# Performance work log

Hardware: AMD Instinct MI355X
Metric: run time of the kernel (lower is better)

The kernel has to match this reference:

```python
import jax, jax.numpy as jnp
import numpy as np

B, N, K = 4, 100000, 128
Q_MIN = 0.5
S_B = 1.0
POT_SCALE = 1.0
REP_SCALE = 1.0
BETA_SCALE = 1.0
E_WEIGHT = 1.0
POS_WEIGHT = 1.0
TIME_WEIGHT = 1.0
HUBER_D = 2.0


def setup_inputs() -> dict:
    key = jax.random.key(0)
    ks = jax.random.split(key, 9)
    return {
        "beta": jax.random.uniform(ks[0], (B, N), dtype=jnp.float32),
        "ccoords": jax.random.normal(ks[1], (B, N, 2), dtype=jnp.float32),
        "pred_energy": jax.random.uniform(ks[2], (B, N), dtype=jnp.float32),
        "pred_pos": jax.random.normal(ks[3], (B, N, 2), dtype=jnp.float32),
        "pred_time": jax.random.uniform(ks[4], (B, N), dtype=jnp.float32),
        "t_energy": jax.random.uniform(ks[5], (B, N), dtype=jnp.float32),
        "t_pos": jax.random.normal(ks[6], (B, N, 2), dtype=jnp.float32),
        "t_time": jax.random.uniform(ks[7], (B, N), dtype=jnp.float32),
        "t_idx": jax.random.randint(ks[8], (B, N), 0, K + 1, dtype=jnp.int32),
    }


def _huber(x, d):
    a = jnp.abs(x)
    return jnp.where(a <= d, 0.5 * x * x, d * (a - 0.5 * d))


def _oc_loss(beta, ccoords, pred_energy, pred_pos, pred_time,
             t_energy, t_pos, t_time, t_idx):
    eps = 1e-4
    beta = jnp.clip(beta, eps, 1.0 - eps)
    q = jnp.arctanh(beta) ** 2 + Q_MIN                     # [B,N]

    obj = t_idx - 1                                        # -1 = noise, 0..K-1 = object id
    M = obj[:, :, None] == jnp.arange(K, dtype=jnp.int32)  # [B,N,K] bool membership
    Mf = M.astype(q.dtype)
    obj_exists = jnp.any(M, axis=1)                        # [B,K]
    exf = obj_exists.astype(q.dtype)

    # condensation point per object = member hit with max charge q (segment argmax)
    q_masked = jnp.where(M, q[:, :, None], -1.0)           # [B,N,K]
    alpha = jnp.argmax(q_masked, axis=1)                   # [B,K]
    x_alpha = jnp.take_along_axis(ccoords, alpha[:, :, None], axis=1)  # [B,K,2]
    q_alpha = jnp.take_along_axis(q, alpha, axis=1)        # [B,K]
    beta_alpha = jnp.take_along_axis(beta, alpha, axis=1)  # [B,K]

    # pairwise hit <-> condensation-point distances, [B,N,K]
    diff = ccoords[:, :, None, :] - x_alpha[:, None, :, :]
    dist = jnp.sqrt(jnp.sum(diff * diff, axis=-1) + 1e-12)

    qq = q[:, :, None] * q_alpha[:, None, :] * exf[:, None, :]
    v_att = qq * (dist * dist) * Mf
    v_rep = qq * jax.nn.relu(1.0 - dist) * (1.0 - Mf)
    n_tot = jnp.asarray(B * N, q.dtype)
    L_att = jnp.sum(v_att) / n_tot
    L_rep = jnp.sum(v_rep) / n_tot

    # beta loss: pull condensation-point betas to 1, suppress noise betas
    n_obj = jnp.maximum(jnp.sum(exf), 1.0)
    L_beta_obj = jnp.sum((1.0 - beta_alpha) * exf) / n_obj
    noise = (t_idx == 0).astype(q.dtype)
    L_noise = jnp.sum(beta * noise) / jnp.maximum(jnp.sum(noise), 1.0)
    L_beta = L_beta_obj + S_B * L_noise

    # payload losses, beta-weighted over non-noise hits
    p = (jnp.arctanh(beta) ** 2) * (1.0 - noise)           # [B,N]
    p_sum = jnp.maximum(jnp.sum(p), 1e-6)
    L_energy = jnp.sum(p * _huber(pred_energy - t_energy, HUBER_D)) / p_sum
    L_pos = jnp.sum(p * jnp.sum((pred_pos - t_pos) ** 2, axis=-1)) / p_sum
    L_time = jnp.sum(p * (pred_time - t_time) ** 2) / p_sum

    return (POT_SCALE * L_att + REP_SCALE * L_rep + BETA_SCALE * L_beta
            + E_WEIGHT * L_energy + POS_WEIGHT * L_pos + TIME_WEIGHT * L_time)


def reference(beta, ccoords, pred_energy, pred_pos, pred_time,
              t_energy, t_pos, t_time, t_idx):
    return _oc_loss(beta, ccoords, pred_energy, pred_pos, pred_time,
                    t_energy, t_pos, t_time, t_idx)
```

## Files before the change

kernel.cpp:

```cpp
#include <hip/hip_runtime.h>
#include <math.h>

#define BB 4
#define NN 100000
#define KK 128
#define HB 256
#define HH 4
#define GX ((NN + HB * HH - 1) / (HB * HH))
#define NBLK (GX * BB)


typedef float v2f __attribute__((ext_vector_type(2)));

#if __has_builtin(__builtin_elementwise_fma)
#define FMA2(a, b, c) __builtin_elementwise_fma((a), (b), (c))
#else
static __device__ __forceinline__ v2f fma2_(v2f a, v2f b, v2f c) {
    v2f r; r.x = __builtin_fmaf(a.x, b.x, c.x); r.y = __builtin_fmaf(a.y, b.y, c.y);
    return r;
}
#define FMA2 fma2_
#endif

#if __has_builtin(__builtin_elementwise_max)
#define MAX2(a, b) __builtin_elementwise_max((a), (b))
#else
static __device__ __forceinline__ v2f max2_(v2f a, v2f b) {
    v2f r; r.x = fmaxf(a.x, b.x); r.y = fmaxf(a.y, b.y);
    return r;
}
#define MAX2 max2_
#endif

__device__ __forceinline__ float clipb(float b) {
    return fminf(fmaxf(b, 1e-4f), 1.0f - 1e-4f);
}

__global__ void k_argmax(const float* __restrict__ beta,
                         const int* __restrict__ tidx,
                         unsigned long long* __restrict__ packed) {
    int b = blockIdx.y;
    __shared__ unsigned long long smax[KK];
    for (int t = threadIdx.x; t < KK; t += blockDim.x) smax[t] = 0ULL;
    __syncthreads();
    const float* betab = beta + b * NN;
    const int*   tib   = tidx + b * NN;
    for (int n = blockIdx.x * blockDim.x + threadIdx.x; n < NN;
         n += gridDim.x * blockDim.x) {
        int obj = tib[n] - 1;
        if (obj >= 0) {
            unsigned hi = __float_as_uint(clipb(betab[n]));
            unsigned long long key = ((unsigned long long)hi << 32) |
                                     (unsigned long long)(0xFFFFFFFFu - (unsigned)n);
            atomicMax(&smax[obj], key);
        }
    }
    __syncthreads();
    for (int t = threadIdx.x; t < KK; t += blockDim.x) {
        unsigned long long v = smax[t];
        if (v) atomicMax(&packed[b * KK + t], v);
    }
}

__global__ void __launch_bounds__(HB) k_main(
    const float*  __restrict__ beta, const float2* __restrict__ cc,
    const float*  __restrict__ pe,   const float2* __restrict__ pp,
    const float*  __restrict__ pt,   const float*  __restrict__ te,
    const float2* __restrict__ tp,   const float*  __restrict__ tt,
    const int*    __restrict__ tidx,
    const unsigned long long* __restrict__ packed,
    float* __restrict__ part) {
    int b = blockIdx.y;
    __shared__ v2f sox[KK / 2];
    __shared__ v2f soy[KK / 2];
    __shared__ v2f soq[KK / 2];
    __shared__ float sred[4][8];
    float* sax = (float*)sox;
    float* say = (float*)soy;
    float* saq = (float*)soq;

    if (threadIdx.x < KK) {
        unsigned long long v = packed[b * KK + threadIdx.x];
        float x = 0.f, y = 0.f, qz = 0.f;
        if (v) {
            unsigned n = 0xFFFFFFFFu - (unsigned)(v & 0xFFFFFFFFu);
            float ba = __uint_as_float((unsigned)(v >> 32));
            float at = atanhf(ba);
            float2 c = cc[b * NN + (int)n];
            x = c.x; y = c.y; qz = at * at + 0.5f;
        }
        sax[threadIdx.x] = x;
        say[threadIdx.x] = y;
        saq[threadIdx.x] = qz;
    }

    int base = blockIdx.x * (HB * HH) + threadIdx.x;
    bool vv[HH]; int ii[HH]; float2 ch[HH]; float rp[HH];
    v2f cx2[HH], cy2[HH];
    #pragma unroll
    for (int h = 0; h < HH; ++h) {
        int n = base + h * HB;
        vv[h] = n < NN;
        ii[h] = b * NN + (vv[h] ? n : 0);
        ch[h] = cc[ii[h]];
        cx2[h].x = ch[h].x; cx2[h].y = ch[h].x;
        cy2[h].x = ch[h].y; cy2[h].y = ch[h].y;
        rp[h] = 0.f;
    }
    __syncthreads();

    const v2f eps2 = {1e-12f, 1e-12f};
    const v2f one2 = {1.0f, 1.0f};
    const v2f zero2 = {0.0f, 0.0f};

    #pragma unroll 2
    for (int k2 = 0; k2 < KK / 2; ++k2) {
        v2f ox = sox[k2], oy = soy[k2], oq = soq[k2];
        #pragma unroll
        for (int h = 0; h < HH; ++h) {
            v2f dx = cx2[h] - ox;
            v2f dy = cy2[h] - oy;
            v2f s  = FMA2(dx, dx, FMA2(dy, dy, eps2));
            v2f d;
            d.x = __builtin_amdgcn_sqrtf(s.x);
            d.y = __builtin_amdgcn_sqrtf(s.y);
            v2f r = MAX2(one2 - d, zero2);
            rp[h] = fmaf(oq.x, r.x, rp[h]);
            rp[h] = fmaf(oq.y, r.y, rp[h]);
        }
    }

    float p_att = 0.f, p_rep = 0.f, p_nb = 0.f, p_nc = 0.f;
    float p_ps = 0.f, p_e = 0.f, p_pos = 0.f, p_tm = 0.f;

    #pragma unroll
    for (int h = 0; h < HH; ++h) {
        if (!vv[h]) continue;
        int   idx = ii[h];
        float rep = rp[h];
        float bc  = clipb(beta[idx]);
        float at  = atanhf(bc);
        float at2 = at * at;
        float q   = at2 + 0.5f;
        int   ti  = tidx[idx];
        int   obj = ti - 1;

        if (obj >= 0) {
            float ox = sax[obj], oy = say[obj], oqz = saq[obj];
            float dx = ch[h].x - ox, dy = ch[h].y - oy;
            float s = fmaf(dx, dx, fmaf(dy, dy, 1e-12f));
            float d = __builtin_amdgcn_sqrtf(s);
            rep   -= oqz * fmaxf(1.0f - d, 0.0f);
            p_att += q * (oqz * s);
        }
        p_rep += q * rep;

        if (ti == 0) {
            p_nb += bc;
            p_nc += 1.0f;
        } else {
            p_ps += at2;
            float de = pe[idx] - te[idx];
            float a  = fabsf(de);
            float hb = (a <= 2.0f) ? (0.5f * de * de) : (2.0f * (a - 1.0f));
            p_e  += at2 * hb;
            float2 ppv = pp[idx], tpv = tp[idx];
            float dpx = ppv.x - tpv.x, dpy = ppv.y - tpv.y;
            p_pos += at2 * (dpx * dpx + dpy * dpy);
            float dt = pt[idx] - tt[idx];
            p_tm += at2 * dt * dt;
        }
    }

    float vals[8] = {p_att, p_rep, p_nb, p_nc, p_ps, p_e, p_pos, p_tm};
    int lane = threadIdx.x & 63, wave = threadIdx.x >> 6;
    #pragma unroll
    for (int i = 0; i < 8; ++i) {
        float v = vals[i];
        #pragma unroll
        for (int off = 32; off > 0; off >>= 1) v += __shfl_down(v, off, 64);
        if (lane == 0) sred[wave][i] = v;
    }
    __syncthreads();
    if (threadIdx.x < 8) {
        float s = sred[0][threadIdx.x] + sred[1][threadIdx.x] +
                  sred[2][threadIdx.x] + sred[3][threadIdx.x];
        part[(b * GX + blockIdx.x) * 8 + threadIdx.x] = s;
    }
}

__global__ void __launch_bounds__(64) k_final(
    const float* __restrict__ part,
    const unsigned long long* __restrict__ packed,
    float* __restrict__ out) {
    int lane = threadIdx.x;

    float nobj = 0.f, sba = 0.f;
    for (int t = lane; t < BB * KK; t += 64) {
        unsigned long long v = packed[t];
        if (v) {
            nobj += 1.f;
            sba  += 1.0f - __uint_as_float((unsigned)(v >> 32));
        }
    }
    #pragma unroll
    for (int off = 32; off > 0; off >>= 1) {
        nobj += __shfl_xor(nobj, off, 64);
        sba  += __shfl_xor(sba, off, 64);
    }

    int comp = lane & 7;
    float v = 0.f;
    for (int r = lane >> 3; r < NBLK; r += 8)
        v += part[r * 8 + comp];
    v += __shfl_xor(v, 8, 64);
    v += __shfl_xor(v, 16, 64);
    v += __shfl_xor(v, 32, 64);
    float tot[8];
    #pragma unroll
    for (int c = 0; c < 8; ++c) tot[c] = __shfl(v, c, 64);

    if (lane == 0) {
        float inv_n  = 1.0f / (float)(BB * NN);
        float L_beta = sba / fmaxf(nobj, 1.0f) +
                       tot[2] / fmaxf(tot[3], 1.0f);
        float p_sum  = fmaxf(tot[4], 1e-6f);
        out[0] = tot[0] * inv_n + tot[1] * inv_n + L_beta +
                 (tot[5] + tot[6] + tot[7]) / p_sum;
    }
}

extern "C" void kernel_launch(void* const* d_in, const int* in_sizes, int n_in,
                              void* d_out, int out_size, void* d_ws, size_t ws_size,
                              hipStream_t stream) {
    const float*  beta = (const float*)d_in[0];
    const float2* cc   = (const float2*)d_in[1];
    const float*  pe   = (const float*)d_in[2];
    const float2* pp   = (const float2*)d_in[3];
    const float*  pt   = (const float*)d_in[4];
    const float*  te   = (const float*)d_in[5];
    const float2* tp   = (const float2*)d_in[6];
    const float*  tt   = (const float*)d_in[7];
    const int*    ti   = (const int*)d_in[8];

    unsigned long long* packed = (unsigned long long*)d_ws;
    float* part = (float*)((char*)d_ws + 4096);
    float* out  = (float*)d_out;

    hipMemsetAsync(packed, 0, 4096, stream);
    k_argmax<<<dim3(64, BB), 256, 0, stream>>>(beta, ti, packed);
    k_main<<<dim3(GX, BB), HB, 0, stream>>>(
        beta, cc, pe, pp, pt, te, tp, tt, ti, packed, part);
    k_final<<<1, 64, 0, stream>>>(part, packed, out);
}
```

Before: 120.1 us.

## Drop memset and final kernel via per-block argmax partials and last-block reduction

The argmax kernel now reads beta and t_idx with vector loads and writes per-block partial maxima instead of doing global atomics. That removes the memset, and the main kernel reduces the 32 partials itself. The separate final kernel is folded into the main kernel through a last-block-done atomic counter. HH rises to 7 with a fixed grid of 56 blocks per batch, giving fewer, larger blocks. The goal is less launch and memset overhead, at the cost of every main block redundantly reducing the partials and of lower parallelism.

Measured after the change: 118.4 us. About the same (-1.4%).

```diff
diff --git a/kernel.cpp b/kernel.cpp
--- a/kernel.cpp
+++ b/kernel.cpp
@@ -5,9 +5,10 @@
 #define NN 100000
 #define KK 128
 #define HB 256
-#define HH 4
-#define GX ((NN + HB * HH - 1) / (HB * HH))
+#define HH 7
+#define GX 56
 #define NBLK (GX * BB)
+#define PB 32
 
 
 typedef float v2f __attribute__((ext_vector_type(2)));
@@ -36,30 +37,35 @@
     return fminf(fmaxf(b, 1e-4f), 1.0f - 1e-4f);
 }
 
-__global__ void k_argmax(const float* __restrict__ beta,
-                         const int* __restrict__ tidx,
-                         unsigned long long* __restrict__ packed) {
+__device__ __forceinline__ unsigned long long mkkey(float bf, unsigned n) {
+    unsigned hi = __float_as_uint(clipb(bf));
+    return ((unsigned long long)hi << 32) |
+           (unsigned long long)(0xFFFFFFFFu - n);
+}
+
+__global__ void __launch_bounds__(256) k_argmax(
+    const float4* __restrict__ beta4, const int4* __restrict__ tidx4,
+    unsigned long long* __restrict__ pk_part, unsigned int* __restrict__ cnt) {
     int b = blockIdx.y;
     __shared__ unsigned long long smax[KK];
-    for (int t = threadIdx.x; t < KK; t += blockDim.x) smax[t] = 0ULL;
-    __syncthreads();
-    const float* betab = beta + b * NN;
-    const int*   tib   = tidx + b * NN;
-    for (int n = blockIdx.x * blockDim.x + threadIdx.x; n < NN;
-         n += gridDim.x * blockDim.x) {
-        int obj = tib[n] - 1;
-        if (obj >= 0) {
-            unsigned hi = __float_as_uint(clipb(betab[n]));
-            unsigned long long key = ((unsigned long long)hi << 32) |
-                                     (unsigned long long)(0xFFFFFFFFu - (unsigned)n);
-            atomicMax(&smax[obj], key);
-        }
-    }
-    __syncthreads();
-    for (int t = threadIdx.x; t < KK; t += blockDim.x) {
-        unsigned long long v = smax[t];
-        if (v) atomicMax(&packed[b * KK + t], v);
-    }
+    for (int t = threadIdx.x; t < KK; t += 256) smax[t] = 0ULL;
+    if (blockIdx.x == 0 && b == 0 && threadIdx.x == 0) *cnt = 0u;
+    __syncthreads();
+    const float4* b4 = beta4 + (size_t)b * (NN / 4);
+    const int4*   t4 = tidx4 + (size_t)b * (NN / 4);
+    for (int i = blockIdx.x * 256 + threadIdx.x; i < NN / 4; i += PB * 256) {
+        float4 bv = b4[i];
+        int4   tv = t4[i];
+        unsigned n0 = 4u * (unsigned)i;
+        if (tv.x > 0) atomicMax(&smax[tv.x - 1], mkkey(bv.x, n0));
+        if (tv.y > 0) atomicMax(&smax[tv.y - 1], mkkey(bv.y, n0 + 1));
+        if (tv.z > 0) atomicMax(&smax[tv.z - 1], mkkey(bv.z, n0 + 2));
+        if (tv.w > 0) atomicMax(&smax[tv.w - 1], mkkey(bv.w, n0 + 3));
+    }
+    __syncthreads();
+    if (threadIdx.x < KK)
+        pk_part[((size_t)b * PB + blockIdx.x) * KK + threadIdx.x] =
+            smax[threadIdx.x];
 }
 
 __global__ void __launch_bounds__(HB) k_main(
@@ -68,19 +74,30 @@
     const float*  __restrict__ pt,   const float*  __restrict__ te,
     const float2* __restrict__ tp,   const float*  __restrict__ tt,
     const int*    __restrict__ tidx,
-    const unsigned long long* __restrict__ packed,
-    float* __restrict__ part) {
+    const unsigned long long* __restrict__ pk_part,
+    unsigned long long* __restrict__ final_packed,
+    float* __restrict__ part, unsigned int* __restrict__ cnt,
+    float* __restrict__ out) {
     int b = blockIdx.y;
     __shared__ v2f sox[KK / 2];
     __shared__ v2f soy[KK / 2];
     __shared__ v2f soq[KK / 2];
     __shared__ float sred[4][8];
+    __shared__ unsigned s_last;
     float* sax = (float*)sox;
     float* say = (float*)soy;
     float* saq = (float*)soq;
 
     if (threadIdx.x < KK) {
-        unsigned long long v = packed[b * KK + threadIdx.x];
+        const unsigned long long* src =
+            pk_part + ((size_t)b * PB) * KK + threadIdx.x;
+        unsigned long long v = 0ULL;
+        #pragma unroll 8
+        for (int pb = 0; pb < PB; ++pb) {
+            unsigned long long u = src[(size_t)pb * KK];
+            v = (u > v) ? u : v;
+        }
+        if (blockIdx.x == 0) final_packed[b * KK + threadIdx.x] = v;
         float x = 0.f, y = 0.f, qz = 0.f;
         if (v) {
             unsigned n = 0xFFFFFFFFu - (unsigned)(v & 0xFFFFFFFFu);
@@ -95,16 +112,16 @@
     }
 
     int base = blockIdx.x * (HB * HH) + threadIdx.x;
-    bool vv[HH]; int ii[HH]; float2 ch[HH]; float rp[HH];
+    bool vv[HH]; int ii[HH]; float rp[HH];
     v2f cx2[HH], cy2[HH];
     #pragma unroll
     for (int h = 0; h < HH; ++h) {
         int n = base + h * HB;
         vv[h] = n < NN;
         ii[h] = b * NN + (vv[h] ? n : 0);
-        ch[h] = cc[ii[h]];
-        cx2[h].x = ch[h].x; cx2[h].y = ch[h].x;
-        cy2[h].x = ch[h].y; cy2[h].y = ch[h].y;
+        float2 c = cc[ii[h]];
+        cx2[h].x = c.x; cx2[h].y = c.x;
+        cy2[h].x = c.y; cy2[h].y = c.y;
         rp[h] = 0.f;
     }
     __syncthreads();
@@ -147,7 +164,7 @@
 
         if (obj >= 0) {
             float ox = sax[obj], oy = say[obj], oqz = saq[obj];
-            float dx = ch[h].x - ox, dy = ch[h].y - oy;
+            float dx = cx2[h].x - ox, dy = cy2[h].x - oy;
             float s = fmaf(dx, dx, fmaf(dy, dy, 1e-12f));
             float d = __builtin_amdgcn_sqrtf(s);
             rep   -= oqz * fmaxf(1.0f - d, 0.0f);
@@ -187,46 +204,53 @@
                   sred[2][threadIdx.x] + sred[3][threadIdx.x];
         part[(b * GX + blockIdx.x) * 8 + threadIdx.x] = s;
     }
-}
-
-__global__ void __launch_bounds__(64) k_final(
-    const float* __restrict__ part,
-    const unsigned long long* __restrict__ packed,
-    float* __restrict__ out) {
-    int lane = threadIdx.x;
-
-    float nobj = 0.f, sba = 0.f;
-    for (int t = lane; t < BB * KK; t += 64) {
-        unsigned long long v = packed[t];
-        if (v) {
-            nobj += 1.f;
-            sba  += 1.0f - __uint_as_float((unsigned)(v >> 32));
-        }
-    }
-    #pragma unroll
-    for (int off = 32; off > 0; off >>= 1) {
-        nobj += __shfl_xor(nobj, off, 64);
-        sba  += __shfl_xor(sba, off, 64);
-    }
-
-    int comp = lane & 7;
-    float v = 0.f;
-    for (int r = lane >> 3; r < NBLK; r += 8)
-        v += part[r * 8 + comp];
-    v += __shfl_xor(v, 8, 64);
-    v += __shfl_xor(v, 16, 64);
-    v += __shfl_xor(v, 32, 64);
-    float tot[8];
-    #pragma unroll
-    for (int c = 0; c < 8; ++c) tot[c] = __shfl(v, c, 64);
-
-    if (lane == 0) {
-        float inv_n  = 1.0f / (float)(BB * NN);
-        float L_beta = sba / fmaxf(nobj, 1.0f) +
-                       tot[2] / fmaxf(tot[3], 1.0f);
-        float p_sum  = fmaxf(tot[4], 1e-6f);
-        out[0] = tot[0] * inv_n + tot[1] * inv_n + L_beta +
-                 (tot[5] + tot[6] + tot[7]) / p_sum;
+    __syncthreads();
+
+    if (threadIdx.x == 0) {
+        __threadfence();
+        unsigned prev = atomicAdd(cnt, 1u);
+        s_last = (prev == (unsigned)(NBLK - 1)) ? 1u : 0u;
+    }
+    __syncthreads();
+    if (s_last) {
+        __threadfence();
+        if (threadIdx.x < 64) {
+            int flane = threadIdx.x;
+
+            float nobj = 0.f, sba = 0.f;
+            for (int t = flane; t < BB * KK; t += 64) {
+                unsigned long long v = final_packed[t];
+                if (v) {
+                    nobj += 1.f;
+                    sba  += 1.0f - __uint_as_float((unsigned)(v >> 32));
+                }
+            }
+            #pragma unroll
+            for (int off = 32; off > 0; off >>= 1) {
+                nobj += __shfl_xor(nobj, off, 64);
+                sba  += __shfl_xor(sba, off, 64);
+            }
+
+            int comp = flane & 7;
+            float v = 0.f;
+            for (int r = flane >> 3; r < NBLK; r += 8)
+                v += part[r * 8 + comp];
+            v += __shfl_xor(v, 8, 64);
+            v += __shfl_xor(v, 16, 64);
+            v += __shfl_xor(v, 32, 64);
+            float tot[8];
+            #pragma unroll
+            for (int c = 0; c < 8; ++c) tot[c] = __shfl(v, c, 64);
+
+            if (flane == 0) {
+                float inv_n  = 1.0f / (float)(BB * NN);
+                float L_beta = sba / fmaxf(nobj, 1.0f) +
+                               tot[2] / fmaxf(tot[3], 1.0f);
+                float p_sum  = fmaxf(tot[4], 1e-6f);
+                out[0] = tot[0] * inv_n + tot[1] * inv_n + L_beta +
+                         (tot[5] + tot[6] + tot[7]) / p_sum;
+            }
+        }
     }
 }
 
@@ -243,13 +267,15 @@
     const float*  tt   = (const float*)d_in[7];
     const int*    ti   = (const int*)d_in[8];
 
-    unsigned long long* packed = (unsigned long long*)d_ws;
-    float* part = (float*)((char*)d_ws + 4096);
-    float* out  = (float*)d_out;
-
-    hipMemsetAsync(packed, 0, 4096, stream);
-    k_argmax<<<dim3(64, BB), 256, 0, stream>>>(beta, ti, packed);
+    unsigned long long* pk_part      = (unsigned long long*)d_ws;
+    unsigned long long* final_packed = (unsigned long long*)((char*)d_ws + 131072);
+    float*              part         = (float*)((char*)d_ws + 135168);
+    unsigned int*       cnt          = (unsigned int*)((char*)d_ws + 147712);
+    float*              out          = (float*)d_out;
+
+    k_argmax<<<dim3(PB, BB), 256, 0, stream>>>(
+        (const float4*)beta, (const int4*)ti, pk_part, cnt);
     k_main<<<dim3(GX, BB), HB, 0, stream>>>(
-        beta, cc, pe, pp, pt, te, tp, tt, ti, packed, part);
-    k_final<<<1, 64, 0, stream>>>(part, packed, out);
-}
+        beta, cc, pe, pp, pt, te, tp, tt, ti,
+        pk_part, final_packed, part, cnt, out);
+}
```
